# Kernel optimization log

Measured on AMD Instinct MI355X. Metric: run time of the kernel, lower is better.

Reference implementation:

```python
import jax, jax.numpy as jnp
import numpy as np

# Problem constants (match init_kwargs)
A = 64          # particles
H = 1024        # hidden width
B = 512         # batch of configurations
V0 = -5.0
SIGMA0 = 0.5
GAUSS_CONST = V0 / (np.sqrt(2.0 * np.pi) * SIGMA0)
INV_2SIG2 = 1.0 / (2.0 * SIGMA0 * SIGMA0)


def setup_inputs() -> dict:
    key = jax.random.key(0)
    ks = jax.random.split(key, 7)
    x = jax.random.normal(ks[0], (B, A), dtype=jnp.float32)
    # 3-layer tanh MLP params: log|psi| = MLP(x) -> scalar
    W1 = jax.random.normal(ks[1], (A, H), dtype=jnp.float32) / np.sqrt(A)
    b1 = jnp.zeros((H,), dtype=jnp.float32)
    W2 = jax.random.normal(ks[2], (H, H), dtype=jnp.float32) / np.sqrt(H)
    b2 = jnp.zeros((H,), dtype=jnp.float32)
    W3 = jax.random.normal(ks[3], (H, 1), dtype=jnp.float32) / np.sqrt(H)
    b3 = jnp.zeros((1,), dtype=jnp.float32)
    return {"x": x, "W1": W1, "b1": b1, "W2": W2, "b2": b2, "W3": W3, "b3": b3}


def _logabs(W1, b1, W2, b2, W3, b3, xs):
    # xs: [A] -> scalar log|psi|
    h = jnp.tanh(xs @ W1 + b1)
    h = jnp.tanh(h @ W2 + b2)
    return (h @ W3 + b3)[0]


def reference(x, W1, b1, W2, b2, W3, b3):
    def logabs(xs):
        return _logabs(W1, b1, W2, b2, W3, b3, xs)

    grad_fn = jax.grad(logabs)  # reverse-mode, like jacrev

    def per_sample(xs):
        g = grad_fn(xs)                       # [A]   dlogabs/dx
        hess = jax.jacrev(grad_fn)(xs)        # [A,A] nested jacrev (backward-over-backward)
        lap = jnp.trace(hess) + jnp.sum(g * g)
        kin = -0.5 * lap
        pot = 0.5 * jnp.sum(xs * xs)
        d = xs[None, :] - xs[:, None]          # [A,A] pairwise differences
        gint = GAUSS_CONST * jnp.sum(jnp.triu(jnp.exp(-(d * d) * INV_2SIG2), k=1))
        return kin + pot + gint

    return jax.vmap(per_sample)(x)  # [B] local energies
```

## Files before the change

kernel.cpp:

```cpp
#include <hip/hip_runtime.h>
#include <hip/hip_bf16.h>
#include <hip/hip_fp8.h>
#include <stdint.h>

#define AN 64
#define HN 1024
#define BN 512
#define GAUSS_CONST (-3.989422804014327f)
#define INV_2SIG2 2.0f

typedef __attribute__((ext_vector_type(8))) short short8;
typedef __attribute__((ext_vector_type(4))) short short4v;
typedef __attribute__((ext_vector_type(4))) float floatx4;

__device__ inline unsigned short f2bf(float f) {
  __hip_bfloat16 h = __float2bfloat16(f);
  return *reinterpret_cast<unsigned short*>(&h);
}

__device__ inline unsigned char f2fp8(float f) {
  __hip_fp8_e4m3 t(f);
  return (unsigned char)t.__x;
}

__device__ inline void gload_lds16(const void* g, void* l) {
  __builtin_amdgcn_global_load_lds(
      (const __attribute__((address_space(1))) void*)g,
      (__attribute__((address_space(3))) void*)l, 16, 0, 0);
}

#define PH_BAR  asm volatile("s_barrier" ::: "memory")
#define WAITV3  asm volatile("s_waitcnt vmcnt(3)" ::: "memory")

__global__ __launch_bounds__(256) void k1(
    const float* __restrict__ x, const float* __restrict__ W1,
    const float* __restrict__ b1, const float* __restrict__ W2,
    unsigned short* __restrict__ h1bf, float* __restrict__ t1f,
    float* __restrict__ a1, float* __restrict__ potgint,
    unsigned char* __restrict__ Pbf8, unsigned short* __restrict__ W2T,
    unsigned short* __restrict__ W2bf, unsigned char* __restrict__ W2T8,
    float* __restrict__ W1T) {
  __shared__ float tile[64][65];
  __shared__ float t1s[HN];
  __shared__ float xs[AN];
  __shared__ float red[4];
  int b = blockIdx.x, tid = threadIdx.x;
  if (b < BN) {
    int s = b;
    if (tid < AN) xs[tid] = x[s * AN + tid];
    __syncthreads();
    #pragma unroll
    for (int cc = 0; cc < 4; ++cc) {
      int j = tid + cc * 256;
      float z = b1[j];
      float cs = 0.f;
      #pragma unroll 8
      for (int a = 0; a < AN; ++a) {
        float wv = W1[a * HN + j];
        z += xs[a] * wv;
        cs += wv * wv;
      }
      float h = tanhf(z), t = 1.f - h * h;
      h1bf[s * HN + j] = f2bf(h);
      t1f[s * HN + j] = t;
      a1[s * HN + j] = cs * h * t;
      t1s[j] = t;
    }
    float val = 0.f;
    #pragma unroll
    for (int p = 0; p < 16; ++p) {
      int idx = tid + p * 256;
      int i = idx >> 6, jj = idx & 63;
      if (jj > i) { float d = xs[i] - xs[jj]; val += __expf(-INV_2SIG2 * d * d); }
    }
    val *= GAUSS_CONST;
    if (tid < AN) val += 0.5f * xs[tid] * xs[tid];
    #pragma unroll
    for (int o = 32; o > 0; o >>= 1) val += __shfl_down(val, o, 64);
    if ((tid & 63) == 0) red[tid >> 6] = val;
    __syncthreads();
    if (tid == 0) potgint[s] = red[0] + red[1] + red[2] + red[3];
    int j4 = tid * 4;
    floatx4 tv = *reinterpret_cast<const floatx4*>(&t1s[j4]);
    size_t outBase = ((size_t)s * 64) * HN + j4;
    for (int a = 0; a < AN; ++a) {
      floatx4 w = *reinterpret_cast<const floatx4*>(&W1[(size_t)a * HN + j4]);
      unsigned p = (unsigned)f2fp8(w[0] * tv[0] * 8.f)
                 | ((unsigned)f2fp8(w[1] * tv[1] * 8.f) << 8)
                 | ((unsigned)f2fp8(w[2] * tv[2] * 8.f) << 16)
                 | ((unsigned)f2fp8(w[3] * tv[3] * 8.f) << 24);
      *reinterpret_cast<unsigned*>(&Pbf8[outBase + (size_t)a * HN]) = p;
    }
  } else if (b < BN + 256) {
    int t = b - BN;
    int jt = (t >> 4) * 64, kt = (t & 15) * 64;
    #pragma unroll
    for (int it = 0; it < 4; ++it) {
      int e = it * 256 + tid;
      int r = e >> 4, cv = (e & 15) * 4;
      floatx4 v = *reinterpret_cast<const floatx4*>(&W2[(size_t)(jt + r) * HN + kt + cv]);
      tile[r][cv] = v[0]; tile[r][cv + 1] = v[1];
      tile[r][cv + 2] = v[2]; tile[r][cv + 3] = v[3];
      short4v o;
      #pragma unroll
      for (int i = 0; i < 4; ++i) o[i] = (short)f2bf(v[i]);
      *reinterpret_cast<short4v*>(&W2bf[(size_t)(jt + r) * HN + kt + cv]) = o;
    }
    __syncthreads();
    #pragma unroll
    for (int it = 0; it < 4; ++it) {
      int e = it * 256 + tid;
      int r = e >> 4, cv = (e & 15) * 4;
      float v0 = tile[cv][r], v1 = tile[cv + 1][r];
      float v2 = tile[cv + 2][r], v3 = tile[cv + 3][r];
      short4v o;
      o[0] = (short)f2bf(v0); o[1] = (short)f2bf(v1);
      o[2] = (short)f2bf(v2); o[3] = (short)f2bf(v3);
      *reinterpret_cast<short4v*>(&W2T[(size_t)(kt + r) * HN + jt + cv]) = o;
      unsigned p8 = (unsigned)f2fp8(v0 * 16.f)
                  | ((unsigned)f2fp8(v1 * 16.f) << 8)
                  | ((unsigned)f2fp8(v2 * 16.f) << 16)
                  | ((unsigned)f2fp8(v3 * 16.f) << 24);
      *reinterpret_cast<unsigned*>(&W2T8[(size_t)(kt + r) * HN + jt + cv]) = p8;
    }
  } else {
    int t = b - (BN + 256);
    int j0 = t * 64;
    #pragma unroll
    for (int it = 0; it < 4; ++it) {
      int e = it * 256 + tid;
      int r = e >> 4, cv = (e & 15) * 4;
      floatx4 v = *reinterpret_cast<const floatx4*>(&W1[(size_t)r * HN + j0 + cv]);
      tile[r][cv] = v[0]; tile[r][cv + 1] = v[1];
      tile[r][cv + 2] = v[2]; tile[r][cv + 3] = v[3];
    }
    __syncthreads();
    #pragma unroll
    for (int it = 0; it < 4; ++it) {
      int e = it * 256 + tid;
      int r = e >> 4, cv = (e & 15) * 4;
      floatx4 o;
      #pragma unroll
      for (int i = 0; i < 4; ++i) o[i] = tile[cv + i][r];
      *reinterpret_cast<floatx4*>(&W1T[(size_t)(j0 + r) * AN + cv]) = o;
    }
  }
}

__global__ __launch_bounds__(256) void k_z2(
    const unsigned short* __restrict__ h1bf, const unsigned short* __restrict__ W2T,
    const float* __restrict__ b2, const float* __restrict__ W3,
    float* __restrict__ dcoef, unsigned short* __restrict__ vbf) {
  __shared__ float redL[4 * 16 * 64];
  int n0 = blockIdx.x * 64, m0 = blockIdx.y * 16;
  int tid = threadIdx.x, w = tid >> 6, l = tid & 63, lr = l & 15, kg = l >> 4;
  floatx4 acc[4];
  #pragma unroll
  for (int nf = 0; nf < 4; ++nf) acc[nf] = (floatx4){0.f, 0.f, 0.f, 0.f};
  int arow = m0 + lr;
  for (int kt = 0; kt < 8; ++kt) {
    int kb = w * 256 + kt * 32 + kg * 8;
    short8 af = *reinterpret_cast<const short8*>(&h1bf[arow * HN + kb]);
    #pragma unroll
    for (int nf = 0; nf < 4; ++nf) {
      short8 bf_ = *reinterpret_cast<const short8*>(&W2T[(n0 + nf * 16 + lr) * HN + kb]);
      acc[nf] = __builtin_amdgcn_mfma_f32_16x16x32_bf16(af, bf_, acc[nf], 0, 0, 0);
    }
  }
  #pragma unroll
  for (int nf = 0; nf < 4; ++nf)
    #pragma unroll
    for (int r = 0; r < 4; ++r)
      redL[w * 1024 + (kg * 4 + r) * 64 + nf * 16 + lr] = acc[nf][r];
  __syncthreads();
  #pragma unroll
  for (int t = 0; t < 4; ++t) {
    int e = tid + t * 256;
    float z = redL[e] + redL[1024 + e] + redL[2048 + e] + redL[3072 + e];
    int row = e >> 6, col = e & 63;
    int s = m0 + row, k2 = n0 + col;
    z += b2[k2];
    float h = tanhf(z), tt = 1.f - h * h, w3 = W3[k2];
    dcoef[s * HN + k2] = -2.f * h * tt * w3;
    vbf[s * HN + k2] = f2bf(tt * w3);
  }
}

__global__ __launch_bounds__(512, 2) void k_bigw(
    const unsigned char* __restrict__ Pbf8,
    const unsigned char* __restrict__ W2T8,
    float* __restrict__ q,
    const unsigned short* __restrict__ vbf, const unsigned short* __restrict__ W2bf,
    float* __restrict__ wbuf) {
  extern __shared__ unsigned char sm8[];
  int bid = blockIdx.x;
  int tid = threadIdx.x;

  if (bid < 512) {
    int xcd = bid & 7, local = bid >> 3;
    int px = local & 3;
    int py = xcd * 16 + (local >> 2);

    int wid = tid >> 6, l = tid & 63;
    int lr = l & 15, kg = l >> 4;
    int wr = wid >> 2, wc = wid & 3;
    int wr128 = wr * 128, wc64 = wc * 64;
    int sl8 = ((kg ^ (((lr >> 2) & 1) << 1)) * 8);

    int srow = tid >> 1;
    int soff = (((tid & 1) ^ ((tid >> 3) & 1)) << 4);
    const unsigned char* aSrc = &Pbf8[(size_t)(py * 256 + srow) * HN + soff];
    const unsigned char* bSrc = &W2T8[(size_t)(px * 256 + srow) * HN + soff];

    auto stA = [&](int slot, int tt, int kh) {
      gload_lds16(aSrc + tt * 64 + kh * 32, &sm8[slot * 16384 + kh * 8192 + tid * 16]);
    };
    auto stB = [&](int buf, int tt, int kh) {
      gload_lds16(bSrc + tt * 64 + kh * 32, &sm8[49152 + buf * 16384 + kh * 8192 + tid * 16]);
    };

    floatx4 acc[8][4];
    #pragma unroll
    for (int m = 0; m < 8; ++m)
      #pragma unroll
      for (int n = 0; n < 4; ++n) acc[m][n] = (floatx4){0.f, 0.f, 0.f, 0.f};

    long af[8], bfr[2];
    auto ldA = [&](int slot, int kh) {
      const unsigned char* Ap = &sm8[slot * 16384 + kh * 8192];
      #pragma unroll
      for (int m = 0; m < 8; ++m)
        af[m] = *reinterpret_cast<const long*>(&Ap[(wr128 + m * 16 + lr) * 32 + sl8]);
    };
    auto ldB = [&](int buf, int kh, int nh) {
      const unsigned char* Bp = &sm8[49152 + buf * 16384 + kh * 8192];
      #pragma unroll
      for (int n = 0; n < 2; ++n)
        bfr[n] = *reinterpret_cast<const long*>(&Bp[(wc64 + (nh * 2 + n) * 16 + lr) * 32 + sl8]);
    };
    auto mm = [&](int nh) {
      __builtin_amdgcn_s_setprio(1);
      #pragma unroll
      for (int m = 0; m < 8; ++m)
        #pragma unroll
        for (int n = 0; n < 2; ++n)
          acc[m][nh * 2 + n] = __builtin_amdgcn_mfma_f32_16x16x32_fp8_fp8(
              af[m], bfr[n], acc[m][nh * 2 + n], 0, 0, 0);
      __builtin_amdgcn_s_setprio(0);
    };

    stA(0, 0, 0); stA(0, 0, 1); stB(0, 0, 0); stB(0, 0, 1);
    stA(1, 1, 0); stA(1, 1, 1);
    WAITV3; PH_BAR;

    int rs = 0;
    for (int t = 0; t < 16; ++t) {
      int rb = t & 1, wb = rb ^ 1;
      int ws = rs + 2; if (ws >= 3) ws -= 3;
      int ta = (t + 2 < 16) ? t + 2 : 15;
      int tb = (t + 1 < 16) ? t + 1 : 15;
      ldA(rs, 0); ldB(rb, 0, 0);
      stB(wb, tb, 0);
      PH_BAR; mm(0); PH_BAR;
      ldB(rb, 0, 1);
      WAITV3;
      PH_BAR; mm(1); PH_BAR;
      ldA(rs, 1); ldB(rb, 1, 0);
      stB(wb, tb, 1); stA(ws, ta, 0); stA(ws, ta, 1);
      PH_BAR; mm(0); PH_BAR;
      ldB(rb, 1, 1);
      WAITV3;
      PH_BAR; mm(1); PH_BAR;
      rs = (rs + 1 == 3) ? 0 : rs + 1;
    }

    int colBase = px * 256 + wc64;
    #pragma unroll
    for (int half = 0; half < 2; ++half) {
      int sOut = py * 4 + wr * 2 + half;
      #pragma unroll
      for (int nf = 0; nf < 4; ++nf) {
        float v = 0.f;
        #pragma unroll
        for (int mf = half * 4; mf < half * 4 + 4; ++mf)
          #pragma unroll
          for (int r = 0; r < 4; ++r) v += acc[mf][nf][r] * acc[mf][nf][r];
        v += __shfl_xor(v, 16, 64);
        v += __shfl_xor(v, 32, 64);
        v *= (1.f / 16384.f);
        if (l < 16) q[(size_t)sOut * HN + colBase + nf * 16 + l] = v;
      }
    }
  } else {
    float* redF = reinterpret_cast<float*>(sm8);
    int wi = bid - 512;
    int m0 = (wi >> 3) * 16, n0 = (wi & 7) * 128;
    int w = tid >> 6, l = tid & 63, lr = l & 15, kg = l >> 4;
    int ks = w >> 1, ch = w & 1;
    floatx4 acc[4];
    #pragma unroll
    for (int nf = 0; nf < 4; ++nf) acc[nf] = (floatx4){0.f, 0.f, 0.f, 0.f};
    int arow = m0 + lr;
    for (int kt = 0; kt < 8; ++kt) {
      int kb = ks * 256 + kt * 32 + kg * 8;
      short8 af = *reinterpret_cast<const short8*>(&vbf[arow * HN + kb]);
      #pragma unroll
      for (int nf = 0; nf < 4; ++nf) {
        short8 bf_ = *reinterpret_cast<const short8*>(
            &W2bf[(size_t)(n0 + ch * 64 + nf * 16 + lr) * HN + kb]);
        acc[nf] = __builtin_amdgcn_mfma_f32_16x16x32_bf16(af, bf_, acc[nf], 0, 0, 0);
      }
    }
    #pragma unroll
    for (int nf = 0; nf < 4; ++nf)
      #pragma unroll
      for (int r = 0; r < 4; ++r)
        redF[w * 1024 + (kg * 4 + r) * 64 + nf * 16 + lr] = acc[nf][r];
    __syncthreads();
    #pragma unroll
    for (int it = 0; it < 4; ++it) {
      int e = it * 512 + tid;
      int row = e >> 7, col = e & 127;
      int ch2 = col >> 6, cc = col & 63;
      float z = redF[(0 * 2 + ch2) * 1024 + row * 64 + cc]
              + redF[(1 * 2 + ch2) * 1024 + row * 64 + cc]
              + redF[(2 * 2 + ch2) * 1024 + row * 64 + cc]
              + redF[(3 * 2 + ch2) * 1024 + row * 64 + cc];
      wbuf[(size_t)(m0 + row) * HN + n0 + col] = z;
    }
  }
}

__global__ __launch_bounds__(256) void k_fin(
    const float* __restrict__ wbuf, const float* __restrict__ a1,
    const float* __restrict__ dcoef, const float* __restrict__ q,
    const float* __restrict__ t1f, const float* __restrict__ W1T,
    const float* __restrict__ potgint, float* __restrict__ out) {
  __shared__ float s_lds[HN];
  __shared__ float gl[256];
  __shared__ float red1[4], red2[4];
  int s = blockIdx.x, tid = threadIdx.x;
  float p1 = 0.f, p2 = 0.f;
  #pragma unroll
  for (int cc = 0; cc < 4; ++cc) {
    int j = tid + cc * 256;
    float wv = wbuf[s * HN + j];
    p1 += a1[s * HN + j] * wv;
    p2 += dcoef[s * HN + j] * q[s * HN + j];
    s_lds[j] = t1f[s * HN + j] * wv;
  }
  __syncthreads();
  int part = tid >> 6, a = tid & 63;
  float gp = 0.f;
  for (int jj = part * 256; jj < part * 256 + 256; ++jj)
    gp += s_lds[jj] * W1T[jj * AN + a];
  gl[tid] = gp;
  #pragma unroll
  for (int o = 32; o > 0; o >>= 1) { p1 += __shfl_down(p1, o, 64); p2 += __shfl_down(p2, o, 64); }
  if ((tid & 63) == 0) { red1[tid >> 6] = p1; red2[tid >> 6] = p2; }
  __syncthreads();
  if (tid < 64) {
    float g = gl[tid] + gl[64 + tid] + gl[128 + tid] + gl[192 + tid];
    float sq = g * g;
    #pragma unroll
    for (int o = 32; o > 0; o >>= 1) sq += __shfl_down(sq, o, 64);
    if (tid == 0) {
      float T1 = -2.f * (red1[0] + red1[1] + red1[2] + red1[3]);
      float T2 = red2[0] + red2[1] + red2[2] + red2[3];
      out[s] = -0.5f * (T1 + T2 + sq) + potgint[s];
    }
  }
}

extern "C" void kernel_launch(void* const* d_in, const int* in_sizes, int n_in,
                              void* d_out, int out_size, void* d_ws, size_t ws_size,
                              hipStream_t stream) {
  const float* x  = (const float*)d_in[0];
  const float* W1 = (const float*)d_in[1];
  const float* b1 = (const float*)d_in[2];
  const float* W2 = (const float*)d_in[3];
  const float* b2 = (const float*)d_in[4];
  const float* W3 = (const float*)d_in[5];
  float* out = (float*)d_out;

  char* ws = (char*)d_ws;
  size_t off = 0;
  auto alloc = [&](size_t bytes) -> void* {
    void* p = ws + off; off += (bytes + 255) & ~(size_t)255; return p;
  };
  unsigned short* W2T  = (unsigned short*)alloc((size_t)HN * HN * 2);
  unsigned short* W2bf = (unsigned short*)alloc((size_t)HN * HN * 2);
  unsigned char*  W2T8 = (unsigned char*)alloc((size_t)HN * HN);
  float*          W1T  = (float*)alloc((size_t)AN * HN * 4);
  unsigned short* h1bf = (unsigned short*)alloc((size_t)BN * HN * 2);
  float*          t1f  = (float*)alloc((size_t)BN * HN * 4);
  float*          a1   = (float*)alloc((size_t)BN * HN * 4);
  float*          dcoef= (float*)alloc((size_t)BN * HN * 4);
  unsigned short* vbf  = (unsigned short*)alloc((size_t)BN * HN * 2);
  float*          wbuf = (float*)alloc((size_t)BN * HN * 4);
  float*          q    = (float*)alloc((size_t)BN * HN * 4);
  float*          pg   = (float*)alloc((size_t)BN * 4);
  unsigned char*  Pbf8 = (unsigned char*)alloc((size_t)BN * AN * HN);

  static bool attrSet = false;
  if (!attrSet) {
    hipFuncSetAttribute((const void*)k_bigw,
                        hipFuncAttributeMaxDynamicSharedMemorySize, 81920);
    attrSet = true;
  }

  k1<<<dim3(BN + 256 + 16), 256, 0, stream>>>(x, W1, b1, W2,
                                              h1bf, t1f, a1, pg,
                                              Pbf8, W2T, W2bf, W2T8, W1T);
  k_z2<<<dim3(HN / 64, BN / 16), 256, 0, stream>>>(h1bf, W2T, b2, W3, dcoef, vbf);
  k_bigw<<<dim3(512 + 256), 512, 81920, stream>>>(Pbf8, W2T8, q, vbf, W2bf, wbuf);
  k_fin<<<dim3(BN), 256, 0, stream>>>(wbuf, a1, dcoef, q, t1f, W1T, pg, out);
}
```

Measured before the change: 179.7 us.

## Permute FP8 K layout for 16-byte LDS fragment reads and halve GEMM barriers

The producer kernel now writes the FP8 operands P and W2T with a permuted K order within each 64-wide chunk. This lets each lane in the FP8 GEMM load a 16-byte fragment that feeds two MFMAs, instead of two separate 8-byte loads. The GEMM main loop is restructured to process full 64-wide K tiles with a new XOR swizzle and fewer barrier phases per iteration, and it adds a final vmcnt(0) wait. The layer-1 loop is also vectorised to four columns per thread, which removes the LDS t1 staging. The risks are correctness of the new permutation and swizzle, and changed overlap between loads and MFMAs.

Result: no change. 177.1 us (-1.5%).

```diff
diff --git a/kernel.cpp b/kernel.cpp
--- a/kernel.cpp
+++ b/kernel.cpp
@@ -12,6 +12,7 @@
 typedef __attribute__((ext_vector_type(8))) short short8;
 typedef __attribute__((ext_vector_type(4))) short short4v;
 typedef __attribute__((ext_vector_type(4))) float floatx4;
+typedef __attribute__((ext_vector_type(2))) long longx2;
 
 __device__ inline unsigned short f2bf(float f) {
   __hip_bfloat16 h = __float2bfloat16(f);
@@ -30,7 +31,12 @@
 }
 
 #define PH_BAR  asm volatile("s_barrier" ::: "memory")
-#define WAITV3  asm volatile("s_waitcnt vmcnt(3)" ::: "memory")
+#define WAITV2  asm volatile("s_waitcnt vmcnt(2)" ::: "memory")
+#define WAITV0  asm volatile("s_waitcnt vmcnt(0)" ::: "memory")
+
+__device__ inline int kperm4(int j) {
+  return (((j >> 3) & 3) << 4) + ((j >> 5) << 3) + (j & 7);
+}
 
 __global__ __launch_bounds__(256) void k1(
     const float* __restrict__ x, const float* __restrict__ W1,
@@ -41,7 +47,6 @@
     unsigned short* __restrict__ W2bf, unsigned char* __restrict__ W2T8,
     float* __restrict__ W1T) {
   __shared__ float tile[64][65];
-  __shared__ float t1s[HN];
   __shared__ float xs[AN];
   __shared__ float red[4];
   int b = blockIdx.x, tid = threadIdx.x;
@@ -49,23 +54,26 @@
     int s = b;
     if (tid < AN) xs[tid] = x[s * AN + tid];
     __syncthreads();
-    #pragma unroll
-    for (int cc = 0; cc < 4; ++cc) {
-      int j = tid + cc * 256;
-      float z = b1[j];
-      float cs = 0.f;
-      #pragma unroll 8
-      for (int a = 0; a < AN; ++a) {
-        float wv = W1[a * HN + j];
-        z += xs[a] * wv;
-        cs += wv * wv;
-      }
-      float h = tanhf(z), t = 1.f - h * h;
-      h1bf[s * HN + j] = f2bf(h);
-      t1f[s * HN + j] = t;
-      a1[s * HN + j] = cs * h * t;
-      t1s[j] = t;
-    }
+    int j4 = tid * 4;
+    floatx4 z4 = *reinterpret_cast<const floatx4*>(&b1[j4]);
+    floatx4 cs4 = (floatx4){0.f, 0.f, 0.f, 0.f};
+    for (int a = 0; a < AN; ++a) {
+      floatx4 w = *reinterpret_cast<const floatx4*>(&W1[(size_t)a * HN + j4]);
+      float xa = xs[a];
+      #pragma unroll
+      for (int e = 0; e < 4; ++e) { z4[e] += xa * w[e]; cs4[e] += w[e] * w[e]; }
+    }
+    floatx4 t4, a4; short4v h4;
+    #pragma unroll
+    for (int e = 0; e < 4; ++e) {
+      float h = tanhf(z4[e]), t = 1.f - h * h;
+      h4[e] = (short)f2bf(h);
+      t4[e] = t;
+      a4[e] = cs4[e] * h * t;
+    }
+    *reinterpret_cast<short4v*>(&h1bf[(size_t)s * HN + j4]) = h4;
+    *reinterpret_cast<floatx4*>(&t1f[(size_t)s * HN + j4]) = t4;
+    *reinterpret_cast<floatx4*>(&a1[(size_t)s * HN + j4]) = a4;
     float val = 0.f;
     #pragma unroll
     for (int p = 0; p < 16; ++p) {
@@ -80,15 +88,14 @@
     if ((tid & 63) == 0) red[tid >> 6] = val;
     __syncthreads();
     if (tid == 0) potgint[s] = red[0] + red[1] + red[2] + red[3];
-    int j4 = tid * 4;
-    floatx4 tv = *reinterpret_cast<const floatx4*>(&t1s[j4]);
-    size_t outBase = ((size_t)s * 64) * HN + j4;
+    int physOff = (j4 & ~63) + kperm4(j4 & 63);
+    size_t outBase = ((size_t)s * 64) * HN + physOff;
     for (int a = 0; a < AN; ++a) {
       floatx4 w = *reinterpret_cast<const floatx4*>(&W1[(size_t)a * HN + j4]);
-      unsigned p = (unsigned)f2fp8(w[0] * tv[0] * 8.f)
-                 | ((unsigned)f2fp8(w[1] * tv[1] * 8.f) << 8)
-                 | ((unsigned)f2fp8(w[2] * tv[2] * 8.f) << 16)
-                 | ((unsigned)f2fp8(w[3] * tv[3] * 8.f) << 24);
+      unsigned p = (unsigned)f2fp8(w[0] * t4[0] * 8.f)
+                 | ((unsigned)f2fp8(w[1] * t4[1] * 8.f) << 8)
+                 | ((unsigned)f2fp8(w[2] * t4[2] * 8.f) << 16)
+                 | ((unsigned)f2fp8(w[3] * t4[3] * 8.f) << 24);
       *reinterpret_cast<unsigned*>(&Pbf8[outBase + (size_t)a * HN]) = p;
     }
   } else if (b < BN + 256) {
@@ -121,7 +128,7 @@
                   | ((unsigned)f2fp8(v1 * 16.f) << 8)
                   | ((unsigned)f2fp8(v2 * 16.f) << 16)
                   | ((unsigned)f2fp8(v3 * 16.f) << 24);
-      *reinterpret_cast<unsigned*>(&W2T8[(size_t)(kt + r) * HN + jt + cv]) = p8;
+      *reinterpret_cast<unsigned*>(&W2T8[(size_t)(kt + r) * HN + jt + kperm4(cv)]) = p8;
     }
   } else {
     int t = b - (BN + 256);
@@ -205,18 +212,24 @@
     int lr = l & 15, kg = l >> 4;
     int wr = wid >> 2, wc = wid & 3;
     int wr128 = wr * 128, wc64 = wc * 64;
-    int sl8 = ((kg ^ (((lr >> 2) & 1) << 1)) * 8);
-
-    int srow = tid >> 1;
-    int soff = (((tid & 1) ^ ((tid >> 3) & 1)) << 4);
-    const unsigned char* aSrc = &Pbf8[(size_t)(py * 256 + srow) * HN + soff];
-    const unsigned char* bSrc = &W2T8[(size_t)(px * 256 + srow) * HN + soff];
-
-    auto stA = [&](int slot, int tt, int kh) {
-      gload_lds16(aSrc + tt * 64 + kh * 32, &sm8[slot * 16384 + kh * 8192 + tid * 16]);
+    int rdOff = ((kg ^ ((lr >> 1) & 3)) << 4);
+
+    int r1 = tid >> 2;
+    int c1 = (tid & 3) ^ ((tid >> 3) & 3);
+    const unsigned char* aSrc = &Pbf8[(size_t)(py * 256 + r1) * HN + c1 * 16];
+    const unsigned char* bSrc = &W2T8[(size_t)(px * 256 + r1) * HN + c1 * 16];
+
+    auto stA = [&](int slot, int tt) {
+      const unsigned char* s = aSrc + tt * 64;
+      unsigned char* d = &sm8[slot * 16384 + tid * 16];
+      gload_lds16(s, d);
+      gload_lds16(s + (size_t)128 * HN, d + 8192);
     };
-    auto stB = [&](int buf, int tt, int kh) {
-      gload_lds16(bSrc + tt * 64 + kh * 32, &sm8[49152 + buf * 16384 + kh * 8192 + tid * 16]);
+    auto stB = [&](int buf, int tt) {
+      const unsigned char* s = bSrc + tt * 64;
+      unsigned char* d = &sm8[49152 + buf * 16384 + tid * 16];
+      gload_lds16(s, d);
+      gload_lds16(s + (size_t)128 * HN, d + 8192);
     };
 
     floatx4 acc[8][4];
@@ -225,54 +238,53 @@
       #pragma unroll
       for (int n = 0; n < 4; ++n) acc[m][n] = (floatx4){0.f, 0.f, 0.f, 0.f};
 
-    long af[8], bfr[2];
-    auto ldA = [&](int slot, int kh) {
-      const unsigned char* Ap = &sm8[slot * 16384 + kh * 8192];
+    longx2 af[8], bfr[2];
+    auto ldA = [&](int slot) {
+      const unsigned char* Ap = &sm8[slot * 16384];
       #pragma unroll
       for (int m = 0; m < 8; ++m)
-        af[m] = *reinterpret_cast<const long*>(&Ap[(wr128 + m * 16 + lr) * 32 + sl8]);
+        af[m] = *reinterpret_cast<const longx2*>(&Ap[(wr128 + m * 16 + lr) * 64 + rdOff]);
     };
-    auto ldB = [&](int buf, int kh, int nh) {
-      const unsigned char* Bp = &sm8[49152 + buf * 16384 + kh * 8192];
+    auto ldB = [&](int buf, int nh) {
+      const unsigned char* Bp = &sm8[49152 + buf * 16384];
       #pragma unroll
       for (int n = 0; n < 2; ++n)
-        bfr[n] = *reinterpret_cast<const long*>(&Bp[(wc64 + (nh * 2 + n) * 16 + lr) * 32 + sl8]);
+        bfr[n] = *reinterpret_cast<const longx2*>(
+            &Bp[(wc64 + (nh * 2 + n) * 16 + lr) * 64 + rdOff]);
     };
     auto mm = [&](int nh) {
       __builtin_amdgcn_s_setprio(1);
       #pragma unroll
       for (int m = 0; m < 8; ++m)
         #pragma unroll
-        for (int n = 0; n < 2; ++n)
+        for (int n = 0; n < 2; ++n) {
           acc[m][nh * 2 + n] = __builtin_amdgcn_mfma_f32_16x16x32_fp8_fp8(
-              af[m], bfr[n], acc[m][nh * 2 + n], 0, 0, 0);
+              af[m].x, bfr[n].x, acc[m][nh * 2 + n], 0, 0, 0);
+          acc[m][nh * 2 + n] = __builtin_amdgcn_mfma_f32_16x16x32_fp8_fp8(
+              af[m].y, bfr[n].y, acc[m][nh * 2 + n], 0, 0, 0);
+        }
       __builtin_amdgcn_s_setprio(0);
     };
 
-    stA(0, 0, 0); stA(0, 0, 1); stB(0, 0, 0); stB(0, 0, 1);
-    stA(1, 1, 0); stA(1, 1, 1);
-    WAITV3; PH_BAR;
+    stA(0, 0); stB(0, 0); stA(1, 1);
+    WAITV2; PH_BAR;
 
     int rs = 0;
     for (int t = 0; t < 16; ++t) {
       int rb = t & 1, wb = rb ^ 1;
       int ws = rs + 2; if (ws >= 3) ws -= 3;
+      int tb = (t + 1 < 16) ? t + 1 : 15;
       int ta = (t + 2 < 16) ? t + 2 : 15;
-      int tb = (t + 1 < 16) ? t + 1 : 15;
-      ldA(rs, 0); ldB(rb, 0, 0);
-      stB(wb, tb, 0);
+      ldA(rs); ldB(rb, 0);
+      stB(wb, tb);
       PH_BAR; mm(0); PH_BAR;
-      ldB(rb, 0, 1);
-      WAITV3;
-      PH_BAR; mm(1); PH_BAR;
-      ldA(rs, 1); ldB(rb, 1, 0);
-      stB(wb, tb, 1); stA(ws, ta, 0); stA(ws, ta, 1);
-      PH_BAR; mm(0); PH_BAR;
-      ldB(rb, 1, 1);
-      WAITV3;
+      ldB(rb, 1);
+      stA(ws, ta);
+      WAITV2;
       PH_BAR; mm(1); PH_BAR;
       rs = (rs + 1 == 3) ? 0 : rs + 1;
     }
+    WAITV0;
 
     int colBase = px * 256 + wc64;
     #pragma unroll
```
